# Optimization experiments

Measured on AMD Instinct MI355X. Metric: run time of the kernel, lower is better.

## Reference

```python
import jax, jax.numpy as jnp
import numpy as np

NEG = -1e9


def _siglu(x):
    return x * jax.nn.sigmoid(x)


def setup_inputs() -> dict:
    key = jax.random.key(0)
    ks = jax.random.split(key, 10)
    B, S, M, D = 2, 2048, 64, 1024
    sc = 0.02
    return {
        "tokens": jax.random.normal(ks[0], (B, S, D), jnp.float32),
        "memory": jax.random.normal(ks[1], (B, M, D), jnp.float32),
        "Wq": jax.random.normal(ks[2], (D, D), jnp.float32) * sc,
        "bq": jnp.zeros((D,), jnp.float32),
        "Wk": jax.random.normal(ks[3], (D, D), jnp.float32) * sc,
        "bk": jnp.zeros((D,), jnp.float32),
        "Wv": jax.random.normal(ks[4], (D, D), jnp.float32) * sc,
        "bv": jnp.zeros((D,), jnp.float32),
        "Wo": jax.random.normal(ks[5], (D, D), jnp.float32) * sc,
        "bo": jnp.zeros((D,), jnp.float32),
        "pool_q": jax.random.normal(ks[6], (M, D), jnp.float32),
        "cell_W": jax.random.normal(ks[7], (2 * D, 2 * D), jnp.float32) * sc,
        "cell_b": jnp.zeros((2 * D,), jnp.float32),
    }


def reference(tokens, memory, Wq, bq, Wk, bk, Wv, bv, Wo, bo, pool_q, cell_W, cell_b):
    B, S, D = tokens.shape
    M = memory.shape[1]
    H = 16
    hd = D // H
    T = M + S

    x = jnp.concatenate([memory, tokens], axis=1)  # (B, T, D)

    # combined causal mask: memory rows/cols fully visible, token block causal
    tok_mask = jnp.triu(jnp.full((S, S), NEG, jnp.float32), k=1)
    mask = jnp.zeros((T, T), jnp.float32).at[M:, M:].set(tok_mask)  # (T, T)

    def heads(w, b):
        return (x @ w.T + b).reshape(B, T, H, hd).transpose(0, 2, 1, 3)

    q = heads(Wq, bq)  # (B, H, T, hd)
    k = heads(Wk, bk)
    v = heads(Wv, bv)

    scores = jnp.einsum("bhqd,bhkd->bhqk", q, k) * (hd ** -0.5) + mask
    attn = jax.nn.softmax(scores, axis=-1)
    ctx = jnp.einsum("bhqk,bhkd->bhqd", attn, v)
    ctx = ctx.transpose(0, 2, 1, 3).reshape(B, T, D)
    attn_out = ctx @ Wo.T + bo

    x = x + attn_out  # residual
    mem_out = x[:, :M]  # (B, M, D)
    tok_out = x[:, M:]  # (B, S, D)

    # attention pooling: one learnable query per memory slot
    pscores = jnp.einsum("md,bsd->bms", pool_q, tok_out) * (D ** -0.5)
    pweights = jax.nn.softmax(pscores, axis=-1)
    summary = jnp.einsum("bms,bsd->bmd", pweights, tok_out)  # (B, M, D)

    # MinimalRNNCell (siglu-gated) applied per memory slot
    combined = jnp.concatenate([mem_out, summary], axis=-1)  # (B, M, 2D)
    update = combined @ cell_W.T + cell_b
    gate, cand = jnp.split(update, 2, axis=-1)
    gate = jax.nn.sigmoid(gate)
    new_memory = mem_out * gate + (1.0 - gate) * _siglu(cand)

    return tok_out, new_memory
```

## Files before the change

### kernel.cpp

```cpp
#include <hip/hip_runtime.h>
#include <hip/hip_bf16.h>

#define B_  2
#define S_  2048
#define M_  64
#define D_  1024
#define T_  2112
#define H_  16
#define HD_ 64
#define BT_ (B_*T_)
#define NEGBIG (-1e9f)
#define LOG2E 1.44269504f

typedef float f32x4  __attribute__((ext_vector_type(4)));
typedef short short8 __attribute__((ext_vector_type(8)));
typedef unsigned short u16x4 __attribute__((ext_vector_type(4)));
typedef __bf16 bf16x8 __attribute__((ext_vector_type(8)));

static __device__ __forceinline__ unsigned short bf16_of(float f) {
  __hip_bfloat16 h = __float2bfloat16(f);
  return __builtin_bit_cast(unsigned short, h);
}

static __device__ __forceinline__ f32x4 mfma_bf16(short8 a, short8 b, f32x4 c) {
  return __builtin_amdgcn_mfma_f32_16x16x32_bf16(
      __builtin_bit_cast(bf16x8, a), __builtin_bit_cast(bf16x8, b), c, 0, 0, 0);
}

static __device__ __forceinline__ void gload16(const void* g, void* lds) {
  __builtin_amdgcn_global_load_lds(
      (const __attribute__((address_space(1))) unsigned int*)g,
      (__attribute__((address_space(3))) unsigned int*)lds, 16, 0, 0);
}


__global__ void k_build_x(const float* __restrict__ tokens,
                          const float* __restrict__ memory,
                          unsigned short* __restrict__ xb) {
  for (int i = blockIdx.x * blockDim.x + threadIdx.x; i < BT_ * D_;
       i += gridDim.x * blockDim.x) {
    int b = i / (T_ * D_);
    int rem = i - b * (T_ * D_);
    int t = rem / D_;
    int d = rem - t * D_;
    float v = (t < M_) ? memory[((size_t)b * M_ + t) * D_ + d]
                       : tokens[((size_t)b * S_ + (t - M_)) * D_ + d];
    xb[i] = bf16_of(v);
  }
}

__global__ void k_cast_all(const float* __restrict__ Wq, const float* __restrict__ Wk,
                           const float* __restrict__ Wv, const float* __restrict__ Wo,
                           const float* __restrict__ cW, const float* __restrict__ pq,
                           unsigned short* __restrict__ Wqkvb, unsigned short* __restrict__ Wob,
                           unsigned short* __restrict__ cWb, unsigned short* __restrict__ pqb) {
  const int NW = D_ * D_;
  const int NC = 4 * D_ * D_;
  const int NP = M_ * D_;
  const int total = 4 * NW + NC + NP;
  for (int i = blockIdx.x * blockDim.x + threadIdx.x; i < total;
       i += gridDim.x * blockDim.x) {
    if (i < 3 * NW) {
      int which = i >> 20, j = i & (NW - 1);
      const float* s = (which == 0) ? Wq : (which == 1) ? Wk : Wv;
      Wqkvb[i] = bf16_of(s[j]);
    } else if (i < 4 * NW) {
      int j = i - 3 * NW;
      Wob[j] = bf16_of(Wo[j]);
    } else if (i < 4 * NW + NC) {
      int j = i - 4 * NW;
      cWb[j] = bf16_of(cW[j]);
    } else {
      int j = i - 4 * NW - NC;
      pqb[j] = bf16_of(pq[j] * 0.03125f * LOG2E);
    }
  }
}

__device__ __forceinline__ void gemm128_core(const unsigned short* __restrict__ A,
                                             const unsigned short* __restrict__ BT,
                                             int K, int m0, int n0,
                                             f32x4 acc[4][4]) {
  __shared__ __align__(16) unsigned short As[2][128][64];
  __shared__ __align__(16) unsigned short Bs[2][128][64];
  const int tid = threadIdx.x;
  const int w = tid >> 6, l = tid & 63;
  const int wr = w >> 1, wc = w & 1;
  const int lr = l & 15, lg = l >> 4;
  f32x4 z; z[0] = z[1] = z[2] = z[3] = 0.f;
#pragma unroll
  for (int i = 0; i < 4; i++)
#pragma unroll
    for (int j = 0; j < 4; j++) acc[i][j] = z;

  auto stage = [&](int buf, int k0) {
#pragma unroll
    for (int c = 0; c < 4; c++) {
      int rbase = c * 32 + w * 8;
      int rr = rbase + (l >> 3);
      int u = (l & 7) ^ (rr & 7);
      gload16(&A[(size_t)(m0 + rr) * K + k0 + u * 8], &As[buf][rbase][0]);
      gload16(&BT[(size_t)(n0 + rr) * K + k0 + u * 8], &Bs[buf][rbase][0]);
    }
  };

  stage(0, 0);
  int cur = 0;
  const int NK = K >> 6;
  for (int kt = 0; kt < NK; kt++) {
    if (kt + 1 < NK) {
      stage(cur ^ 1, (kt + 1) << 6);
      asm volatile("s_waitcnt vmcnt(8)" ::: "memory");
    } else {
      asm volatile("s_waitcnt vmcnt(0)" ::: "memory");
    }
    __builtin_amdgcn_s_barrier();

    short8 a[4][2], b[4][2];
#pragma unroll
    for (int i = 0; i < 4; i++) {
      int row = wr * 64 + i * 16 + lr;
      int sw = row & 7;
#pragma unroll
      for (int kk = 0; kk < 2; kk++)
        a[i][kk] = *(const short8*)&As[cur][row][(((kk << 2) | lg) ^ sw) * 8];
    }
#pragma unroll
    for (int j = 0; j < 4; j++) {
      int row = wc * 64 + j * 16 + lr;
      int sw = row & 7;
#pragma unroll
      for (int kk = 0; kk < 2; kk++)
        b[j][kk] = *(const short8*)&Bs[cur][row][(((kk << 2) | lg) ^ sw) * 8];
    }
    __builtin_amdgcn_s_setprio(1);
#pragma unroll
    for (int kk = 0; kk < 2; kk++)
#pragma unroll
      for (int i = 0; i < 4; i++)
#pragma unroll
        for (int j = 0; j < 4; j++)
          acc[i][j] = mfma_bf16(a[i][kk], b[j][kk], acc[i][j]);
    __builtin_amdgcn_s_setprio(0);

    __builtin_amdgcn_s_barrier();
    cur ^= 1;
  }
}

__device__ __forceinline__ void gemm_core(const unsigned short* __restrict__ A,
                                          const unsigned short* __restrict__ BT,
                                          int ldk, int Klen, int m0, int n0,
                                          f32x4 acc[4]) {
  __shared__ __align__(16) unsigned short As[64][40];
  __shared__ __align__(16) unsigned short Bs[64][40];
  const int tid = threadIdx.x;
  const int w = tid >> 6, l = tid & 63;
  const int sr = tid >> 2, sc = (tid & 3) * 8;
  f32x4 z; z[0] = z[1] = z[2] = z[3] = 0.f;
  acc[0] = acc[1] = acc[2] = acc[3] = z;
  for (int k0 = 0; k0 < Klen; k0 += 32) {
    __syncthreads();
    *(short8*)&As[sr][sc] = *(const short8*)&A[(size_t)(m0 + sr) * ldk + k0 + sc];
    *(short8*)&Bs[sr][sc] = *(const short8*)&BT[(size_t)(n0 + sr) * ldk + k0 + sc];
    __syncthreads();
    short8 a = *(const short8*)&As[w * 16 + (l & 15)][(l >> 4) * 8];
#pragma unroll
    for (int n = 0; n < 4; n++) {
      short8 b = *(const short8*)&Bs[n * 16 + (l & 15)][(l >> 4) * 8];
      acc[n] = mfma_bf16(a, b, acc[n]);
    }
  }
}

__global__ __launch_bounds__(256) void k_qkv(
    const unsigned short* __restrict__ xb, const unsigned short* __restrict__ Wqkvb,
    const float* __restrict__ bq, const float* __restrict__ bk,
    const float* __restrict__ bv, unsigned short* __restrict__ qg,
    unsigned short* __restrict__ kg, unsigned short* __restrict__ vTg) {
  const int which = blockIdx.x >> 3;
  const unsigned short* W = Wqkvb + (size_t)which * D_ * D_;
  const float* bias = (which == 0) ? bq : ((which == 1) ? bk : bv);
  f32x4 acc[4][4];
  const int m0 = blockIdx.y * 128, n0 = (blockIdx.x & 7) * 128;
  gemm128_core(xb, W, D_, m0, n0, acc);
  const int tid = threadIdx.x, w = tid >> 6, l = tid & 63;
  const int wr = w >> 1, wc = w & 1;
#pragma unroll
  for (int i = 0; i < 4; i++) {
#pragma unroll
    for (int j = 0; j < 4; j++) {
#pragma unroll
      for (int r = 0; r < 4; r++) {
        int m = m0 + wr * 64 + i * 16 + (l >> 4) * 4 + r;
        int c = n0 + wc * 64 + j * 16 + (l & 15);
        int b = (m >= T_) ? 1 : 0;
        int t = m - b * T_;
        int h = c >> 6, dh = c & 63;
        int bh = b * H_ + h;
        float v = acc[i][j][r] + bias[c];
        if (which == 0)
          qg[((size_t)bh * T_ + t) * HD_ + dh] = bf16_of(v * 0.125f * LOG2E);
        else if (which == 1)
          kg[((size_t)bh * T_ + t) * HD_ + dh] = bf16_of(v);
        else
          vTg[((size_t)bh * HD_ + dh) * T_ + t] = bf16_of(v);
      }
    }
  }
}

__global__ __launch_bounds__(256) void k_attn(
    const unsigned short* __restrict__ qg, const unsigned short* __restrict__ kg,
    const unsigned short* __restrict__ vTg, unsigned short* __restrict__ ctx) {
  const int id = blockIdx.x;
  const int xcd = id & 7;
  const int rem = id >> 3;
  const int g = rem / 33, qtr = rem - g * 33;
  const int qt = (qtr == 0) ? 0 : 33 - qtr;
  const int bh = g * 8 + xcd;
  const int tid = threadIdx.x, w = tid >> 6, l = tid & 63;
  const int lr = l & 15, lg = l >> 4;
  __shared__ __align__(16) unsigned short Ks[2][64][64];
  __shared__ __align__(16) unsigned short Vs[2][64][64];
  __shared__ __align__(16) unsigned short Ps[4][16][72];

  const unsigned short* qb = qg + (size_t)bh * T_ * HD_;
  const unsigned short* kb = kg + (size_t)bh * T_ * HD_;
  const unsigned short* vb = vTg + (size_t)bh * HD_ * T_;

  short8 aq[2];
  const int qrow = qt * 64 + w * 16 + lr;
#pragma unroll
  for (int st = 0; st < 2; st++)
    aq[st] = *(const short8*)&qb[(size_t)qrow * HD_ + st * 32 + lg * 8];

  f32x4 zz; zz[0] = zz[1] = zz[2] = zz[3] = 0.f;
  f32x4 o[4];
  o[0] = o[1] = o[2] = o[3] = zz;
  float mrun = -1e30f, lrun = 0.f;

  const int nkt = (qt == 0) ? 33 : qt + 1;

  auto stage = [&](int buf, int kb2) {
#pragma unroll
    for (int i = 0; i < 2; i++) {
      int rr = w * 16 + i * 8 + (l >> 3);
      int swz = ((l & 7) ^ (rr & 7)) * 8;
      gload16(&kb[(size_t)(kb2 + rr) * HD_ + swz], &Ks[buf][w * 16 + i * 8][0]);
      gload16(&vb[(size_t)rr * T_ + kb2 + swz], &Vs[buf][w * 16 + i * 8][0]);
    }
  };

  stage(0, 0);
  __syncthreads();
  int cur = 0;

  for (int j = 0; j < nkt; j++) {
    const int kbase = j * 64;
    if (j + 1 < nkt) stage(cur ^ 1, kbase + 64);

    short8 bkf[2][4];
#pragma unroll
    for (int n = 0; n < 4; n++) {
      int row = n * 16 + lr;
      int sw = lr & 7;
#pragma unroll
      for (int st = 0; st < 2; st++)
        bkf[st][n] = *(const short8*)&Ks[cur][row][((st * 4 + lg) ^ sw) * 8];
    }
    f32x4 s[4];
    s[0] = s[1] = s[2] = s[3] = zz;
    __builtin_amdgcn_s_setprio(1);
#pragma unroll
    for (int st = 0; st < 2; st++)
#pragma unroll
      for (int n = 0; n < 4; n++)
        s[n] = mfma_bf16(bkf[st][n], aq[st], s[n]);
    __builtin_amdgcn_s_setprio(0);

    if (qt > 0 && j == qt) {
      const int tql = w * 16 + lr;
#pragma unroll
      for (int n = 0; n < 4; n++)
#pragma unroll
        for (int r = 0; r < 4; r++) {
          int tkl = n * 16 + lg * 4 + r;
          if (tkl > tql) s[n][r] = NEGBIG;
        }
    }
    float pm = s[0][0];
#pragma unroll
    for (int n = 0; n < 4; n++)
#pragma unroll
      for (int r = 0; r < 4; r++) pm = fmaxf(pm, s[n][r]);
    pm = fmaxf(pm, __shfl_xor(pm, 16));
    pm = fmaxf(pm, __shfl_xor(pm, 32));

    if (__any(pm > mrun + 8.f)) {
      float mn = fmaxf(mrun, pm);
      float fac = exp2f(mrun - mn);
      mrun = mn;
      lrun *= fac;
      float fr[4];
#pragma unroll
      for (int r = 0; r < 4; r++) fr[r] = __shfl(fac, lg * 4 + r);
#pragma unroll
      for (int n = 0; n < 4; n++)
#pragma unroll
        for (int r = 0; r < 4; r++) o[n][r] *= fr[r];
    }
#pragma unroll
    for (int n = 0; n < 4; n++) {
      u16x4 pk;
#pragma unroll
      for (int r = 0; r < 4; r++) {
        float p = exp2f(s[n][r] - mrun);
        lrun += p;
        pk[r] = bf16_of(p);
      }
      *(u16x4*)&Ps[w][lr][n * 16 + lg * 4] = pk;
    }

    short8 bvf[2][4];
#pragma unroll
    for (int n = 0; n < 4; n++) {
      int row = n * 16 + lr;
      int sw = lr & 7;
#pragma unroll
      for (int st = 0; st < 2; st++)
        bvf[st][n] = *(const short8*)&Vs[cur][row][((st * 4 + lg) ^ sw) * 8];
    }
    short8 ap[2];
#pragma unroll
    for (int st = 0; st < 2; st++)
      ap[st] = *(const short8*)&Ps[w][lr][st * 32 + lg * 8];
    __builtin_amdgcn_s_setprio(1);
#pragma unroll
    for (int st = 0; st < 2; st++)
#pragma unroll
      for (int n = 0; n < 4; n++)
        o[n] = mfma_bf16(ap[st], bvf[st][n], o[n]);
    __builtin_amdgcn_s_setprio(0);

    __syncthreads();
    cur ^= 1;
  }
  lrun += __shfl_xor(lrun, 16);
  lrun += __shfl_xor(lrun, 32);
  float linv[4];
#pragma unroll
  for (int r = 0; r < 4; r++) linv[r] = 1.f / __shfl(lrun, lg * 4 + r);

  const int b = bh >> 4, h = bh & 15;
#pragma unroll
  for (int n = 0; n < 4; n++)
#pragma unroll
    for (int r = 0; r < 4; r++) {
      int tq = qt * 64 + w * 16 + lg * 4 + r;
      float val = o[n][r] * linv[r];
      ctx[((size_t)(b * T_ + tq)) * D_ + h * HD_ + n * 16 + lr] = bf16_of(val);
    }
}

__global__ __launch_bounds__(256) void k_out(
    const unsigned short* __restrict__ ctxb, const unsigned short* __restrict__ Wob,
    const float* __restrict__ bo, const float* __restrict__ tokens,
    const float* __restrict__ memory, float* __restrict__ out_tok,
    unsigned short* __restrict__ tokb, unsigned short* __restrict__ tokTb,
    float* __restrict__ memout, unsigned short* __restrict__ comb) {
  f32x4 acc[4][4];
  const int m0 = blockIdx.y * 128, n0 = blockIdx.x * 128;
  gemm128_core(ctxb, Wob, D_, m0, n0, acc);
  const int tid = threadIdx.x, w = tid >> 6, l = tid & 63;
  const int wr = w >> 1, wc = w & 1;
#pragma unroll
  for (int i = 0; i < 4; i++) {
#pragma unroll
    for (int j = 0; j < 4; j++) {
#pragma unroll
      for (int r = 0; r < 4; r++) {
        int m = m0 + wr * 64 + i * 16 + (l >> 4) * 4 + r;
        int c = n0 + wc * 64 + j * 16 + (l & 15);
        int b = (m >= T_) ? 1 : 0;
        int t = m - b * T_;
        float xo = (t < M_) ? memory[((size_t)b * M_ + t) * D_ + c]
                            : tokens[((size_t)b * S_ + (t - M_)) * D_ + c];
        float val = acc[i][j][r] + bo[c] + xo;
        if (t < M_) {
          memout[((size_t)b * M_ + t) * D_ + c] = val;
          comb[((size_t)b * M_ + t) * (2 * D_) + c] = bf16_of(val);
        } else {
          size_t ti = (size_t)b * S_ + (t - M_);
          out_tok[ti * D_ + c] = val;
          tokb[ti * D_ + c] = bf16_of(val);
          tokTb[((size_t)b * D_ + c) * S_ + (t - M_)] = bf16_of(val);
        }
      }
    }
  }
}

__global__ __launch_bounds__(256) void k_pscore_part(
    const unsigned short* __restrict__ pqb, const unsigned short* __restrict__ tokb,
    float* __restrict__ pscp) {
  const int stile = blockIdx.x, ks = blockIdx.y, b = blockIdx.z;
  f32x4 acc[4];
  gemm_core(pqb + ks * 256, tokb + (size_t)b * S_ * D_ + ks * 256, D_, 256,
            0, stile * 64, acc);
  const int tid = threadIdx.x, w = tid >> 6, l = tid & 63;
  float* dst = pscp + ((size_t)(ks * B_ + b) * M_) * S_;
#pragma unroll
  for (int n = 0; n < 4; n++) {
#pragma unroll
    for (int r = 0; r < 4; r++) {
      int m = w * 16 + (l >> 4) * 4 + r;
      int s = stile * 64 + n * 16 + (l & 15);
      dst[(size_t)m * S_ + s] = acc[n][r];
    }
  }
}

__global__ __launch_bounds__(256) void k_psoftmax(const float* __restrict__ pscp,
                                                  unsigned short* __restrict__ pw) {
  const int row = blockIdx.x;
  const int b = row >> 6, m = row & 63;
  const int tid = threadIdx.x;
  float v[8];
  float mx = -1e30f;
#pragma unroll
  for (int i = 0; i < 8; i++) {
    int s = tid + i * 256;
    float acc = 0.f;
#pragma unroll
    for (int ks = 0; ks < 4; ks++)
      acc += pscp[((size_t)(ks * B_ + b) * M_ + m) * S_ + s];
    v[i] = acc;
    mx = fmaxf(mx, acc);
  }
#pragma unroll
  for (int off = 1; off < 64; off <<= 1) mx = fmaxf(mx, __shfl_xor(mx, off));
  __shared__ float rm[4], rs[4];
  if ((tid & 63) == 0) rm[tid >> 6] = mx;
  __syncthreads();
  mx = fmaxf(fmaxf(rm[0], rm[1]), fmaxf(rm[2], rm[3]));
  float sum = 0.f;
#pragma unroll
  for (int i = 0; i < 8; i++) {
    v[i] = exp2f(v[i] - mx);
    sum += v[i];
  }
#pragma unroll
  for (int off = 1; off < 64; off <<= 1) sum += __shfl_xor(sum, off);
  if ((tid & 63) == 0) rs[tid >> 6] = sum;
  __syncthreads();
  float inv = 1.f / (rs[0] + rs[1] + rs[2] + rs[3]);
#pragma unroll
  for (int i = 0; i < 8; i++)
    pw[(size_t)row * S_ + tid + i * 256] = bf16_of(v[i] * inv);
}

__global__ __launch_bounds__(256) void k_summary_part(
    const unsigned short* __restrict__ pw, const unsigned short* __restrict__ tokTb,
    float* __restrict__ sump) {
  const int nt = blockIdx.x, ks = blockIdx.y, b = blockIdx.z;
  f32x4 acc[4];
  gemm_core(pw + (size_t)b * M_ * S_ + ks * 256,
            tokTb + (size_t)b * D_ * S_ + ks * 256, S_, 256, 0, nt * 64, acc);
  const int tid = threadIdx.x, w = tid >> 6, l = tid & 63;
  float* dst = sump + ((size_t)(ks * B_ + b) * M_) * D_;
#pragma unroll
  for (int n = 0; n < 4; n++) {
#pragma unroll
    for (int r = 0; r < 4; r++) {
      int m = w * 16 + (l >> 4) * 4 + r;
      int c = nt * 64 + n * 16 + (l & 15);
      dst[(size_t)m * D_ + c] = acc[n][r];
    }
  }
}

__global__ void k_sumcomb(const float* __restrict__ sump,
                          unsigned short* __restrict__ comb) {
  int i = blockIdx.x * blockDim.x + threadIdx.x;
  if (i >= B_ * M_ * D_) return;
  int bm = i >> 10, c = i & 1023;
  int b = bm >> 6, m = bm & 63;
  float acc = 0.f;
#pragma unroll
  for (int ks = 0; ks < 8; ks++)
    acc += sump[((size_t)(ks * B_ + b) * M_ + m) * D_ + c];
  comb[((size_t)b * M_ + m) * (2 * D_) + D_ + c] = bf16_of(acc);
}

__global__ __launch_bounds__(256) void k_cell_part(
    const unsigned short* __restrict__ comb, const unsigned short* __restrict__ cWb,
    float* __restrict__ cellp) {
  const int nt = blockIdx.x, mt = blockIdx.y, ks = blockIdx.z;
  f32x4 acc[4];
  gemm_core(comb + ks * 512, cWb + ks * 512, 2 * D_, 512, mt * 64, nt * 64, acc);
  const int tid = threadIdx.x, w = tid >> 6, l = tid & 63;
#pragma unroll
  for (int n = 0; n < 4; n++) {
#pragma unroll
    for (int r = 0; r < 4; r++) {
      int m = mt * 64 + w * 16 + (l >> 4) * 4 + r;
      int c = nt * 64 + n * 16 + (l & 15);
      cellp[((size_t)ks * (B_ * M_) + m) * (2 * D_) + c] = acc[n][r];
    }
  }
}

__global__ void k_newmem(const float* __restrict__ cellp,
                         const float* __restrict__ cb,
                         const float* __restrict__ memout,
                         float* __restrict__ out2) {
  int i = blockIdx.x * blockDim.x + threadIdx.x;
  if (i >= B_ * M_ * D_) return;
  int r = i >> 10, d = i & 1023;
  float gsum = cb[d], csum = cb[D_ + d];
#pragma unroll
  for (int ks = 0; ks < 4; ks++) {
    gsum += cellp[((size_t)ks * (B_ * M_) + r) * (2 * D_) + d];
    csum += cellp[((size_t)ks * (B_ * M_) + r) * (2 * D_) + D_ + d];
  }
  float sg = 1.f / (1.f + __expf(-gsum));
  float sc = 1.f / (1.f + __expf(-csum));
  out2[i] = memout[i] * sg + (1.f - sg) * (csum * sc);
}

extern "C" void kernel_launch(void* const* d_in, const int* in_sizes, int n_in,
                              void* d_out, int out_size, void* d_ws, size_t ws_size,
                              hipStream_t stream) {
  const float* tokens = (const float*)d_in[0];
  const float* memory = (const float*)d_in[1];
  const float* Wq = (const float*)d_in[2];
  const float* bq = (const float*)d_in[3];
  const float* Wk = (const float*)d_in[4];
  const float* bk = (const float*)d_in[5];
  const float* Wv = (const float*)d_in[6];
  const float* bv = (const float*)d_in[7];
  const float* Wo = (const float*)d_in[8];
  const float* bo = (const float*)d_in[9];
  const float* pool_q = (const float*)d_in[10];
  const float* cell_W = (const float*)d_in[11];
  const float* cell_b = (const float*)d_in[12];

  size_t off = 0;
  auto alloc = [&](size_t bytes) -> void* {
    void* p = (char*)d_ws + off;
    off += (bytes + 255) & ~(size_t)255;
    return p;
  };
  unsigned short* xb    = (unsigned short*)alloc((size_t)BT_ * D_ * 2);
  unsigned short* Wqkvb = (unsigned short*)alloc((size_t)3 * D_ * D_ * 2);
  unsigned short* Wob   = (unsigned short*)alloc((size_t)D_ * D_ * 2);
  unsigned short* cWb   = (unsigned short*)alloc((size_t)(2 * D_) * (2 * D_) * 2);
  unsigned short* pqb   = (unsigned short*)alloc((size_t)M_ * D_ * 2);
  unsigned short* qg    = (unsigned short*)alloc((size_t)B_ * H_ * T_ * HD_ * 2);
  unsigned short* kg    = (unsigned short*)alloc((size_t)B_ * H_ * T_ * HD_ * 2);
  unsigned short* vTg   = (unsigned short*)alloc((size_t)B_ * H_ * HD_ * T_ * 2);
  unsigned short* ctxb  = (unsigned short*)alloc((size_t)BT_ * D_ * 2);
  unsigned short* tokb  = (unsigned short*)alloc((size_t)B_ * S_ * D_ * 2);
  unsigned short* tokTb = (unsigned short*)alloc((size_t)B_ * D_ * S_ * 2);
  float*          memout= (float*)alloc((size_t)B_ * M_ * D_ * 4);
  unsigned short* comb  = (unsigned short*)alloc((size_t)B_ * M_ * 2 * D_ * 2);
  unsigned short* pwt   = (unsigned short*)alloc((size_t)B_ * M_ * S_ * 2);
  float*          pscp  = (float*)alloc((size_t)4 * B_ * M_ * S_ * 4);
  float*          sump  = (float*)alloc((size_t)8 * B_ * M_ * D_ * 4);
  float*          cellp = (float*)alloc((size_t)4 * B_ * M_ * 2 * D_ * 4);

  float* out_tok = (float*)d_out;
  float* out_mem = out_tok + (size_t)B_ * S_ * D_;

  k_build_x<<<2048, 256, 0, stream>>>(tokens, memory, xb);
  k_cast_all<<<4096, 256, 0, stream>>>(Wq, Wk, Wv, Wo, cell_W, pool_q,
                                       Wqkvb, Wob, cWb, pqb);

  k_qkv<<<dim3(24, 33), 256, 0, stream>>>(xb, Wqkvb, bq, bk, bv, qg, kg, vTg);
  k_attn<<<1056, 256, 0, stream>>>(qg, kg, vTg, ctxb);
  k_out<<<dim3(8, 33), 256, 0, stream>>>(ctxb, Wob, bo, tokens, memory, out_tok,
                                         tokb, tokTb, memout, comb);
  k_pscore_part<<<dim3(32, 4, 2), 256, 0, stream>>>(pqb, tokb, pscp);
  k_psoftmax<<<B_ * M_, 256, 0, stream>>>(pscp, pwt);
  k_summary_part<<<dim3(16, 8, 2), 256, 0, stream>>>(pwt, tokTb, sump);
  k_sumcomb<<<512, 256, 0, stream>>>(sump, comb);
  k_cell_part<<<dim3(32, 2, 4), 256, 0, stream>>>(comb, cWb, cellp);
  k_newmem<<<512, 256, 0, stream>>>(cellp, cell_b, memout, out_mem);
}
```

Baseline: 223.2 us.

## Rewrite QKV GEMM with 192x256 tiles, 512 threads, direct-to-LDS swizzled loads

Replaces the shared 128x128 GEMM core in the QKV projection with a dedicated 192x256 tile kernel using 8 waves, K-step 64, and XOR-swizzled LDS layout filled via direct global-to-LDS 16-byte loads. Each wave now computes a 96x64 sub-tile, which raises MFMA work per LDS read and cuts the block count from 792 to 264. Priority hints are set around the MFMA bursts. The risks are higher register pressure from 24 accumulators and a less even spread of 264 blocks across the CUs. Loads and compute are also not overlapped, since the loop waits on every stage.

```diff
diff --git a/kernel.cpp b/kernel.cpp
--- a/kernel.cpp
+++ b/kernel.cpp
@@ -173,27 +173,84 @@
   }
 }
 
-__global__ __launch_bounds__(256) void k_qkv(
+__global__ __launch_bounds__(512, 2) void k_qkv(
     const unsigned short* __restrict__ xb, const unsigned short* __restrict__ Wqkvb,
     const float* __restrict__ bq, const float* __restrict__ bk,
     const float* __restrict__ bv, unsigned short* __restrict__ qg,
     unsigned short* __restrict__ kg, unsigned short* __restrict__ vTg) {
-  const int which = blockIdx.x >> 3;
-  const unsigned short* W = Wqkvb + (size_t)which * D_ * D_;
+  __shared__ __align__(16) unsigned short As[192][64];
+  __shared__ __align__(16) unsigned short Bs[256][64];
+  const int tid = threadIdx.x;
+  const int w = tid >> 6, l = tid & 63;
+  const int wr = w >> 2, wc = w & 3;
+  const int lr = l & 15, lg = l >> 4;
+  const int m0 = blockIdx.y * 192;
+  const int n0 = blockIdx.x * 256;
+  const int which = blockIdx.x >> 2;
   const float* bias = (which == 0) ? bq : ((which == 1) ? bk : bv);
-  f32x4 acc[4][4];
-  const int m0 = blockIdx.y * 128, n0 = (blockIdx.x & 7) * 128;
-  gemm128_core(xb, W, D_, m0, n0, acc);
-  const int tid = threadIdx.x, w = tid >> 6, l = tid & 63;
-  const int wr = w >> 1, wc = w & 1;
-#pragma unroll
-  for (int i = 0; i < 4; i++) {
+
+  f32x4 acc[6][4];
+  f32x4 z; z[0] = z[1] = z[2] = z[3] = 0.f;
+#pragma unroll
+  for (int i = 0; i < 6; i++)
+#pragma unroll
+    for (int j = 0; j < 4; j++) acc[i][j] = z;
+
+  auto stage = [&](int k0) {
+#pragma unroll
+    for (int t = 0; t < 7; t++) {
+      int g = w * 7 + t;
+      if (g < 24) {
+        int r0 = g * 8;
+        int rr = r0 + (l >> 3);
+        int u = (l & 7) ^ (rr & 7);
+        gload16(&xb[(size_t)(m0 + rr) * D_ + k0 + u * 8], &As[r0][0]);
+      } else {
+        int r0 = (g - 24) * 8;
+        int rr = r0 + (l >> 3);
+        int u = (l & 7) ^ (rr & 7);
+        gload16(&Wqkvb[(size_t)(n0 + rr) * D_ + k0 + u * 8], &Bs[r0][0]);
+      }
+    }
+  };
+
+  for (int kt = 0; kt < D_ / 64; kt++) {
+    stage(kt << 6);
+    asm volatile("s_waitcnt vmcnt(0)" ::: "memory");
+    __builtin_amdgcn_s_barrier();
+#pragma unroll
+    for (int kk = 0; kk < 2; kk++) {
+      short8 a[6], b[4];
+#pragma unroll
+      for (int i = 0; i < 6; i++) {
+        int row = wr * 96 + i * 16 + lr;
+        a[i] = *(const short8*)&As[row][(((kk << 2) | lg) ^ (row & 7)) * 8];
+      }
+#pragma unroll
+      for (int j = 0; j < 4; j++) {
+        int row = wc * 64 + j * 16 + lr;
+        b[j] = *(const short8*)&Bs[row][(((kk << 2) | lg) ^ (row & 7)) * 8];
+      }
+      __builtin_amdgcn_s_setprio(1);
+#pragma unroll
+      for (int i = 0; i < 6; i++)
+#pragma unroll
+        for (int j = 0; j < 4; j++)
+          acc[i][j] = mfma_bf16(a[i], b[j], acc[i][j]);
+      __builtin_amdgcn_s_setprio(0);
+    }
+    __builtin_amdgcn_s_barrier();
+  }
+
+#pragma unroll
+  for (int i = 0; i < 6; i++) {
 #pragma unroll
     for (int j = 0; j < 4; j++) {
 #pragma unroll
       for (int r = 0; r < 4; r++) {
-        int m = m0 + wr * 64 + i * 16 + (l >> 4) * 4 + r;
-        int c = n0 + wc * 64 + j * 16 + (l & 15);
+        int m = m0 + wr * 96 + i * 16 + lg * 4 + r;
+        int cg = n0 + wc * 64 + j * 16 + lr;
+        int c = cg & 1023;
         int b = (m >= T_) ? 1 : 0;
         int t = m - b * T_;
         int h = c >> 6, dh = c & 63;
@@ -577,7 +634,7 @@
   k_cast_all<<<4096, 256, 0, stream>>>(Wq, Wk, Wv, Wo, cell_W, pool_q,
                                        Wqkvb, Wob, cWb, pqb);
 
-  k_qkv<<<dim3(24, 33), 256, 0, stream>>>(xb, Wqkvb, bq, bk, bv, qg, kg, vTg);
+  k_qkv<<<dim3(12, 22), 512, 0, stream>>>(xb, Wqkvb, bq, bk, bv, qg, kg, vTg);
   k_attn<<<1056, 256, 0, stream>>>(qg, kg, vTg, ctxb);
   k_out<<<dim3(8, 33), 256, 0, stream>>>(ctxb, Wob, bo, tokens, memory, out_tok,
                                          tokb, tokTb, memout, comb);
```

Result: slower. 251.2 us, median of 2 (+12.5%).

## Single-buffer V tile and split K/V waits with vmcnt barriers in attention

Applied to the files above, without the earlier changes.

The attention kernel now keeps a single V tile in shared memory instead of a double buffer. Each iteration loads the current V tile, prefetches the next K tile, and waits with explicit vmcnt counts, so the QK^T and softmax work can proceed before V arrives. This cuts LDS use, which may allow more blocks per CU, and replaces __syncthreads with raw s_barrier calls. In exchange V latency is only overlapped with the softmax of the same tile, and correctness depends on the hand-counted vmcnt values matching the gload16 instruction count.

```diff
diff --git a/kernel.cpp b/kernel.cpp
--- a/kernel.cpp
+++ b/kernel.cpp
@@ -222,7 +222,7 @@
   const int tid = threadIdx.x, w = tid >> 6, l = tid & 63;
   const int lr = l & 15, lg = l >> 4;
   __shared__ __align__(16) unsigned short Ks[2][64][64];
-  __shared__ __align__(16) unsigned short Vs[2][64][64];
+  __shared__ __align__(16) unsigned short Vs[64][64];
   __shared__ __align__(16) unsigned short Ps[4][16][72];
 
   const unsigned short* qb = qg + (size_t)bh * T_ * HD_;
@@ -242,23 +242,37 @@
 
   const int nkt = (qt == 0) ? 33 : qt + 1;
 
-  auto stage = [&](int buf, int kb2) {
+  const int srow8 = w * 16 + (l >> 3);
+  const int ldrow8 = w * 16 + ((l >> 3) & ~0u);
+  auto stageK = [&](int buf, int kb2) {
 #pragma unroll
     for (int i = 0; i < 2; i++) {
-      int rr = w * 16 + i * 8 + (l >> 3);
+      int rr = srow8 + i * 8;
       int swz = ((l & 7) ^ (rr & 7)) * 8;
       gload16(&kb[(size_t)(kb2 + rr) * HD_ + swz], &Ks[buf][w * 16 + i * 8][0]);
-      gload16(&vb[(size_t)rr * T_ + kb2 + swz], &Vs[buf][w * 16 + i * 8][0]);
     }
   };
-
-  stage(0, 0);
-  __syncthreads();
+  auto stageV = [&](int kb2) {
+#pragma unroll
+    for (int i = 0; i < 2; i++) {
+      int rr = srow8 + i * 8;
+      int swz = ((l & 7) ^ (rr & 7)) * 8;
+      gload16(&vb[(size_t)rr * T_ + kb2 + swz], &Vs[w * 16 + i * 8][0]);
+    }
+  };
+
+  stageK(0, 0);
   int cur = 0;
 
   for (int j = 0; j < nkt; j++) {
     const int kbase = j * 64;
-    if (j + 1 < nkt) stage(cur ^ 1, kbase + 64);
+    const bool more = (j + 1 < nkt);
+    stageV(kbase);
+    if (more) stageK(cur ^ 1, kbase + 64);
+
+    if (more) asm volatile("s_waitcnt vmcnt(4)" ::: "memory");
+    else      asm volatile("s_waitcnt vmcnt(2)" ::: "memory");
+    __builtin_amdgcn_s_barrier();
 
     short8 bkf[2][4];
 #pragma unroll
@@ -322,6 +336,10 @@
       *(u16x4*)&Ps[w][lr][n * 16 + lg * 4] = pk;
     }
 
+    if (more) asm volatile("s_waitcnt vmcnt(2)" ::: "memory");
+    else      asm volatile("s_waitcnt vmcnt(0)" ::: "memory");
+    __builtin_amdgcn_s_barrier();
+
     short8 bvf[2][4];
 #pragma unroll
     for (int n = 0; n < 4; n++) {
@@ -329,7 +347,7 @@
       int sw = lr & 7;
 #pragma unroll
       for (int st = 0; st < 2; st++)
-        bvf[st][n] = *(const short8*)&Vs[cur][row][((st * 4 + lg) ^ sw) * 8];
+        bvf[st][n] = *(const short8*)&Vs[row][((st * 4 + lg) ^ sw) * 8];
     }
     short8 ap[2];
 #pragma unroll
@@ -343,7 +361,7 @@
         o[n] = mfma_bf16(ap[st], bvf[st][n], o[n]);
     __builtin_amdgcn_s_setprio(0);
 
-    __syncthreads();
+    __builtin_amdgcn_s_barrier();
     cur ^= 1;
   }
   lrun += __shfl_xor(lrun, 16);
```

New measurement: 237.1 us. 6.2% more time.
